# Performance work log

Hardware: AMD Instinct MI355X
Metric: run time of the kernel (lower is better)

Reference implementation:

```python
import jax, jax.numpy as jnp
import numpy as np

B, S, D, H = 2, 2048, 1024, 16
HD = D // H
EPS = 1e-5


def layer_norm(x, g, b):
    m = jnp.mean(x, axis=-1, keepdims=True)
    v = jnp.mean(jnp.square(x - m), axis=-1, keepdims=True)
    return (x - m) * jax.lax.rsqrt(v + EPS) * g + b


def setup_inputs() -> dict:
    key = jax.random.key(0)
    ks = jax.random.split(key, 16)
    s = 0.02
    x = jax.random.normal(ks[0], (B, S, D), dtype=jnp.float32)
    mask = jax.random.randint(ks[1], (1, 1, S, S), 0, 2, dtype=jnp.int32)
    return {
        "x": x,
        "mask": mask,
        "Wq": jax.random.normal(ks[2], (D, D), jnp.float32) * s,
        "Wk": jax.random.normal(ks[3], (D, D), jnp.float32) * s,
        "Wv": jax.random.normal(ks[4], (D, D), jnp.float32) * s,
        "Wo": jax.random.normal(ks[5], (D, D), jnp.float32) * s,
        "bo": jax.random.normal(ks[6], (D,), jnp.float32) * s,
        "ln1_g": jnp.ones((D,), jnp.float32),
        "ln1_b": jnp.zeros((D,), jnp.float32),
        "W1": jax.random.normal(ks[7], (D, 4 * D), jnp.float32) * s,
        "b1": jax.random.normal(ks[8], (4 * D,), jnp.float32) * s,
        "W2": jax.random.normal(ks[9], (4 * D, D), jnp.float32) * s,
        "b2": jax.random.normal(ks[10], (D,), jnp.float32) * s,
        "ln2_g": jnp.ones((D,), jnp.float32),
        "ln2_b": jnp.zeros((D,), jnp.float32),
    }


def reference(x, mask, Wq, Wk, Wv, Wo, bo, ln1_g, ln1_b, W1, b1, W2, b2, ln2_g, ln2_b):
    # --- multi-head attention (dropout = identity in eval) ---
    q = (x @ Wq).reshape(B, S, H, HD)
    k = (x @ Wk).reshape(B, S, H, HD)
    v = (x @ Wv).reshape(B, S, H, HD)
    scores = jnp.einsum("bshd,bthd->bhst", q, k) / jnp.sqrt(jnp.float32(HD))
    scores = jnp.where(mask == 1, jnp.float32(-1e9), scores)
    p = jax.nn.softmax(scores, axis=-1)
    o = jnp.einsum("bhst,bthd->bshd", p, v).reshape(B, S, D)
    attn_out = o @ Wo + bo
    # --- residual with norm on the branch (note: norm applied to attn output) ---
    x = x + layer_norm(attn_out, ln1_g, ln1_b)
    # --- FFN: gelu after fc1 AND after fc2 (as in source) ---
    h = jax.nn.gelu(x @ W1 + b1, approximate=False)
    h = jax.nn.gelu(h @ W2 + b2, approximate=False)
    x = x + layer_norm(h, ln2_g, ln2_b)
    return x
```

## Files before the change

### kernel.cpp

```cpp
#include <hip/hip_runtime.h>
#include <hip/hip_bf16.h>
#include <cstdint>

#define BB 2
#define SS 2048
#define DD 1024
#define HH 16
#define HDIM 64
#define MROWS (BB*SS)

typedef __bf16 bf16;
using bf16x8 = __bf16 __attribute__((ext_vector_type(8)));
using bf16x4 = __bf16 __attribute__((ext_vector_type(4)));
using bf16x2 = __bf16 __attribute__((ext_vector_type(2)));
using f32x4  = float __attribute__((ext_vector_type(4)));

__device__ __forceinline__ float gelu_exact(float x) {
    return 0.5f * x * (1.f + erff(x * 0.70710678118654752f));
}

__device__ __forceinline__ void stage16(const bf16* g, bf16* lds_chunk_base, int lane) {
#if __has_builtin(__builtin_amdgcn_global_load_lds)
    __builtin_amdgcn_global_load_lds((const __attribute__((address_space(1))) void*)g,
                                     (__attribute__((address_space(3))) void*)lds_chunk_base,
                                     16, 0, 0);
#else
    *(bf16x8*)(lds_chunk_base + lane * 8) = *(const bf16x8*)g;
#endif
}

__global__ __launch_bounds__(256) void prep_kernel(
    const float* __restrict__ x, bf16* __restrict__ x_b,
    const int* __restrict__ mask, unsigned long long* __restrict__ maskb,
    const float* __restrict__ Wq, const float* __restrict__ Wk,
    const float* __restrict__ Wv, const float* __restrict__ Wo,
    const float* __restrict__ W1, const float* __restrict__ W2,
    bf16* __restrict__ Wqkv_t, bf16* __restrict__ Wo_t,
    bf16* __restrict__ W1_t, bf16* __restrict__ W2_t) {
    const int bid = blockIdx.x;
    if (bid < 4096) {
        int i = bid * 256 + threadIdx.x;
        float4 v = ((const float4*)x)[i];
        bf16x4 o;
        o[0] = (bf16)v.x; o[1] = (bf16)v.y; o[2] = (bf16)v.z; o[3] = (bf16)v.w;
        *(bf16x4*)(x_b + (size_t)i * 4) = o;
        return;
    }
    if (bid < 20480) {
        int gid = (bid - 4096) * 256 + threadIdx.x;
        int mv = mask[gid];
        unsigned long long bal = __ballot(mv == 1);
        if ((threadIdx.x & 63) == 0) maskb[gid >> 6] = bal;
        return;
    }
    int t = bid - 20480;
    const float* W; bf16* Wt; int K, N, bx, by;
    if (t < 4096) {
        int wsel = t >> 10;
        int tt = t & 1023;
        W  = (wsel == 0) ? Wq : (wsel == 1) ? Wk : (wsel == 2) ? Wv : Wo;
        Wt = (wsel == 3) ? Wo_t : (Wqkv_t + (size_t)wsel * 1024 * 1024);
        K = 1024; N = 1024; bx = (tt & 31) * 32; by = (tt >> 5) * 32;
    } else if (t < 8192) {
        int tt = t - 4096;
        W = W1; Wt = W1_t; K = 1024; N = 4096;
        bx = (tt & 127) * 32; by = (tt >> 7) * 32;
    } else {
        int tt = t - 8192;
        W = W2; Wt = W2_t; K = 4096; N = 1024;
        bx = (tt & 31) * 32; by = (tt >> 5) * 32;
    }
    __shared__ float tile[32][33];
    int tx = threadIdx.x & 31;
    int ty = threadIdx.x >> 5;
#pragma unroll
    for (int j = 0; j < 4; ++j)
        tile[ty + j * 8][tx] = W[(size_t)(by + ty + j * 8) * N + bx + tx];
    __syncthreads();
#pragma unroll
    for (int j = 0; j < 4; ++j)
        Wt[(size_t)(bx + ty + j * 8) * K + by + tx] = (bf16)tile[tx][ty + j * 8];
}

template <int EPI>
__global__ __launch_bounds__(256, 3) void gemm_bt(const bf16* __restrict__ A,
                                                  const bf16* __restrict__ Bt,
                                                  void* __restrict__ C,
                                                  void* __restrict__ C2,
                                                  const float* __restrict__ bias,
                                                  int M, int N, int K, int ldk) {
    __shared__ __align__(16) bf16 As[128 * 64];
    __shared__ __align__(16) bf16 Bs[128 * 64];
    const int tid  = threadIdx.x;
    const int lane = tid & 63;
    const int wave = tid >> 6;
    const int l16  = lane & 15;
    const int quad = lane >> 4;
    const int wm = wave >> 1, wn = wave & 1;
    const int m0 = blockIdx.y * 128, n0 = blockIdx.x * 128;
    const int z  = blockIdx.z;
    A  += (size_t)z * K;
    Bt += (size_t)z * K;

    f32x4 acc[4][4];
#pragma unroll
    for (int i = 0; i < 4; ++i)
#pragma unroll
        for (int j = 0; j < 4; ++j) acc[i][j] = (f32x4){0.f, 0.f, 0.f, 0.f};

    const int nsteps = K >> 6;
    for (int kt = 0; kt < nsteps; ++kt) {
        const int kbase = kt << 6;
#pragma unroll
        for (int c = 0; c < 4; ++c) {
            int chunk = wave * 4 + c;
            int gi = chunk * 64 + lane;
            int m  = gi >> 3;
            int cp = gi & 7;
            int g  = cp ^ (m & 7);
            stage16(A  + (size_t)(m0 + m) * ldk + kbase + g * 8, As + chunk * 512, lane);
            stage16(Bt + (size_t)(n0 + m) * ldk + kbase + g * 8, Bs + chunk * 512, lane);
        }
        __syncthreads();
#pragma unroll
        for (int ks = 0; ks < 2; ++ks) {
            bf16x8 af[4], bfr[4];
#pragma unroll
            for (int i = 0; i < 4; ++i) {
                int m = wm * 64 + i * 16 + l16;
                int g = ks * 4 + quad;
                af[i]  = *(const bf16x8*)(As + m * 64 + ((g ^ (m & 7)) * 8));
                int n = wn * 64 + i * 16 + l16;
                bfr[i] = *(const bf16x8*)(Bs + n * 64 + ((g ^ (n & 7)) * 8));
            }
#pragma unroll
            for (int i = 0; i < 4; ++i)
#pragma unroll
                for (int j = 0; j < 4; ++j)
                    acc[i][j] = __builtin_amdgcn_mfma_f32_16x16x32_bf16(af[i], bfr[j], acc[i][j], 0, 0, 0);
        }
        __syncthreads();
    }

    float* Cz = (EPI == 4) ? (z ? (float*)C2 : (float*)C) : nullptr;
#pragma unroll
    for (int i = 0; i < 4; ++i) {
        int row = m0 + wm * 64 + i * 16 + quad * 4;
#pragma unroll
        for (int j = 0; j < 4; ++j) {
            int col = n0 + wn * 64 + j * 16 + l16;
            float bv = (EPI == 2) ? bias[col] : 0.f;
#pragma unroll
            for (int r = 0; r < 4; ++r) {
                float v = acc[i][j][r];
                if (EPI == 2) v = gelu_exact(v + bv);
                size_t idx = (size_t)(row + r) * N + col;
                if (EPI == 4) Cz[idx] = v;
                else          ((bf16*)C)[idx] = (bf16)v;
            }
        }
    }
}

__global__ __launch_bounds__(256) void flash_attn(const bf16* __restrict__ qkv,
                                                  const unsigned long long* __restrict__ maskb,
                                                  bf16* __restrict__ o) {
    __shared__ __align__(16) bf16 Ks[128 * 64];
    __shared__ __align__(16) bf16 Vts[64 * 136];
    const int tid  = threadIdx.x;
    const int lane = tid & 63;
    const int wave = tid >> 6;
    const int l16  = lane & 15;
    const int quad = lane >> 4;
    const int bh = blockIdx.y;
    const int b = bh >> 4, h = bh & 15;
    const int q0 = blockIdx.x * 64;
    const size_t rowb = (size_t)b * SS;
    const float SCL = 0.18033688011112042f;

    const size_t qrow = (rowb + q0 + wave * 16 + l16) * 3072 + h * 64;
    bf16x8 qf[2];
    qf[0] = *(const bf16x8*)(qkv + qrow + quad * 8);
    qf[1] = *(const bf16x8*)(qkv + qrow + 32 + quad * 8);

    f32x4 oacc[4];
#pragma unroll
    for (int d = 0; d < 4; ++d) oacc[d] = (f32x4){0.f, 0.f, 0.f, 0.f};
    float lsum = 0.f;
    const int mrow32 = (q0 + wave * 16 + l16) * 32;

    const int vt_tc = (lane >> 4) * 32 + ((lane >> 1) & 3) * 8 + ((lane >> 3) & 1) * 4 + 2 * (lane & 1);

    for (int kt = 0; kt < SS / 128; ++kt) {
        const int t0 = kt * 128;
        ulonglong2 mw = *(const ulonglong2*)(maskb + mrow32 + kt * 2);
        __syncthreads();
#pragma unroll
        for (int c = 0; c < 4; ++c) {
            int chunk = wave * 4 + c;
            int gi = chunk * 64 + lane;
            int t  = gi >> 3;
            int cp = gi & 7;
            int g  = cp ^ (t & 7);
            stage16(qkv + (rowb + t0 + t) * 3072 + 1024 + h * 64 + g * 8, Ks + chunk * 512, lane);
        }
#pragma unroll
        for (int c = 0; c < 2; ++c) {
            int d8 = (wave + 4 * c) * 8;
            const bf16* vg = qkv + (rowb + t0 + 2 * lane) * 3072 + 2048 + h * 64 + d8;
            bf16x8 v0 = *(const bf16x8*)(vg);
            bf16x8 v1 = *(const bf16x8*)(vg + 3072);
#pragma unroll
            for (int j = 0; j < 8; ++j) {
                bf16x2 pr; pr[0] = v0[j]; pr[1] = v1[j];
                *(bf16x2*)(Vts + (d8 + j) * 136 + vt_tc) = pr;
            }
        }
        __syncthreads();

        f32x4 st[8];
#pragma unroll
        for (int tg = 0; tg < 8; ++tg) {
            int tl = tg * 16 + l16;
            bf16x8 a0 = *(const bf16x8*)(Ks + tl * 64 + ((quad       ^ (tl & 7)) * 8));
            bf16x8 a1 = *(const bf16x8*)(Ks + tl * 64 + (((4 + quad) ^ (tl & 7)) * 8));
            f32x4 s = (f32x4){0.f, 0.f, 0.f, 0.f};
            s = __builtin_amdgcn_mfma_f32_16x16x32_bf16(a0, qf[0], s, 0, 0, 0);
            s = __builtin_amdgcn_mfma_f32_16x16x32_bf16(a1, qf[1], s, 0, 0, 0);
            st[tg] = s;
        }
        unsigned long long s0 = mw.x >> (quad * 4);
        unsigned long long s1 = mw.y >> (quad * 4);
        bf16x8 pva[4];
#pragma unroll
        for (int tg = 0; tg < 8; ++tg) {
            unsigned int bits = (unsigned int)(((tg < 4) ? s0 : s1) >> ((tg & 3) * 16));
#pragma unroll
            for (int r = 0; r < 4; ++r) {
                float p = __builtin_amdgcn_exp2f(st[tg][r] * SCL);
                p = ((bits >> r) & 1u) ? 0.f : p;
                lsum += p;
                pva[tg >> 1][(tg & 1) * 4 + r] = (bf16)p;
            }
        }
#pragma unroll
        for (int kc = 0; kc < 4; ++kc) {
#pragma unroll
            for (int dg = 0; dg < 4; ++dg) {
                bf16x8 bfrag = *(const bf16x8*)(Vts + (dg * 16 + l16) * 136 + kc * 32 + quad * 8);
                oacc[dg] = __builtin_amdgcn_mfma_f32_16x16x32_bf16(pva[kc], bfrag, oacc[dg], 0, 0, 0);
            }
        }
    }

    lsum += __shfl_xor(lsum, 16, 64);
    lsum += __shfl_xor(lsum, 32, 64);
#pragma unroll
    for (int r = 0; r < 4; ++r) {
        float lr = __shfl(lsum, quad * 4 + r, 64);
        float inv_l = 1.f / lr;
        bf16* orow = o + (rowb + q0 + wave * 16 + quad * 4 + r) * DD + h * 64;
#pragma unroll
        for (int dg = 0; dg < 4; ++dg)
            orow[dg * 16 + l16] = (bf16)(oacc[dg][r] * inv_l);
    }
}

template <bool GELU, bool WB16>
__global__ __launch_bounds__(256) void ln_fused(const float* __restrict__ resid,
                                                const float* __restrict__ p0,
                                                const float* __restrict__ p1,
                                                const float* __restrict__ bias,
                                                const float* __restrict__ g,
                                                const float* __restrict__ bb,
                                                float* __restrict__ outf,
                                                bf16* __restrict__ outb) {
    const int row = blockIdx.x;
    const int tid = threadIdx.x;
    const size_t base = (size_t)row * DD + tid * 4;
    float4 a0 = *(const float4*)(p0 + base);
    float4 a1 = *(const float4*)(p1 + base);
    float4 bz = *(const float4*)(bias + tid * 4);
    float ax = a0.x + a1.x + bz.x;
    float ay = a0.y + a1.y + bz.y;
    float az = a0.z + a1.z + bz.z;
    float aw = a0.w + a1.w + bz.w;
    if (GELU) { ax = gelu_exact(ax); ay = gelu_exact(ay); az = gelu_exact(az); aw = gelu_exact(aw); }
    float s1 = ax + ay + az + aw;
    float s2 = ax * ax + ay * ay + az * az + aw * aw;
#pragma unroll
    for (int off = 32; off; off >>= 1) {
        s1 += __shfl_xor(s1, off, 64);
        s2 += __shfl_xor(s2, off, 64);
    }
    __shared__ float red[8];
    if ((tid & 63) == 0) { red[(tid >> 6) * 2] = s1; red[(tid >> 6) * 2 + 1] = s2; }
    __syncthreads();
    s1 = red[0] + red[2] + red[4] + red[6];
    s2 = red[1] + red[3] + red[5] + red[7];
    float mean = s1 * (1.f / DD);
    float var  = s2 * (1.f / DD) - mean * mean;
    float rs = rsqrtf(var + 1e-5f);
    float4 gv = *(const float4*)(g + tid * 4);
    float4 bv = *(const float4*)(bb + tid * 4);
    float4 rv = *(const float4*)(resid + base);
    float y0 = rv.x + (ax - mean) * rs * gv.x + bv.x;
    float y1 = rv.y + (ay - mean) * rs * gv.y + bv.y;
    float y2 = rv.z + (az - mean) * rs * gv.z + bv.z;
    float y3 = rv.w + (aw - mean) * rs * gv.w + bv.w;
    float4 yo = make_float4(y0, y1, y2, y3);
    *(float4*)(outf + base) = yo;
    if (WB16) {
        bf16x4 ob;
        ob[0] = (bf16)y0; ob[1] = (bf16)y1; ob[2] = (bf16)y2; ob[3] = (bf16)y3;
        *(bf16x4*)(outb + base) = ob;
    }
}

extern "C" void kernel_launch(void* const* d_in, const int* in_sizes, int n_in,
                              void* d_out, int out_size, void* d_ws, size_t ws_size,
                              hipStream_t stream) {
    const float* x    = (const float*)d_in[0];
    const int*   mask = (const int*)d_in[1];
    const float* Wq   = (const float*)d_in[2];
    const float* Wk   = (const float*)d_in[3];
    const float* Wv   = (const float*)d_in[4];
    const float* Wo   = (const float*)d_in[5];
    const float* bo   = (const float*)d_in[6];
    const float* ln1g = (const float*)d_in[7];
    const float* ln1b = (const float*)d_in[8];
    const float* W1   = (const float*)d_in[9];
    const float* b1   = (const float*)d_in[10];
    const float* W2   = (const float*)d_in[11];
    const float* b2   = (const float*)d_in[12];
    const float* ln2g = (const float*)d_in[13];
    const float* ln2b = (const float*)d_in[14];

    char* w = (char*)d_ws;
    bf16* Wqkv_t = (bf16*)w; w += (size_t)3072 * 1024 * 2;
    bf16* Wo_t   = (bf16*)w; w += (size_t)1024 * 1024 * 2;
    bf16* W1_t   = (bf16*)w; w += (size_t)4096 * 1024 * 2;
    bf16* W2_t   = (bf16*)w; w += (size_t)1024 * 4096 * 2;
    bf16* x_b    = (bf16*)w; w += (size_t)MROWS * DD * 2;
    bf16* qkv    = (bf16*)w; w += (size_t)MROWS * 3072 * 2;
    float* R     = (float*)w; w += (size_t)MROWS * DD * 8;
    float* x1_f  = (float*)w; w += (size_t)MROWS * DD * 4;
    unsigned long long* maskb = (unsigned long long*)w; w += (size_t)SS * 32 * 8;
    bf16* o_b  = x_b;
    bf16* x1_b = x_b;
    float* op0 = R;
    float* op1 = R + (size_t)MROWS * DD;
    bf16*  h_b = (bf16*)R;
    float* fp0 = (float*)d_out;
    float* fp1 = (float*)qkv;

    prep_kernel<<<32768, 256, 0, stream>>>(x, x_b, mask, maskb,
                                           Wq, Wk, Wv, Wo, W1, W2,
                                           Wqkv_t, Wo_t, W1_t, W2_t);

    gemm_bt<0><<<dim3(24, 32, 1), 256, 0, stream>>>(x_b, Wqkv_t, qkv, nullptr, nullptr, MROWS, 3072, 1024, 1024);
    flash_attn<<<dim3(SS / 64, BB * HH), 256, 0, stream>>>(qkv, maskb, o_b);
    gemm_bt<4><<<dim3(8, 32, 2), 256, 0, stream>>>(o_b, Wo_t, op0, op1, nullptr, MROWS, 1024, 512, 1024);
    ln_fused<false, true><<<MROWS, 256, 0, stream>>>(x, op0, op1, bo, ln1g, ln1b, x1_f, x1_b);
    gemm_bt<2><<<dim3(32, 32, 1), 256, 0, stream>>>(x1_b, W1_t, h_b, nullptr, b1, MROWS, 4096, 1024, 1024);
    gemm_bt<4><<<dim3(8, 32, 2), 256, 0, stream>>>(h_b, W2_t, fp0, fp1, nullptr, MROWS, 1024, 2048, 4096);
    ln_fused<true, false><<<MROWS, 256, 0, stream>>>(x1_f, fp0, fp1, b2, ln2g, ln2b, (float*)d_out, nullptr);
}
```

Baseline: 390.7 us.

## Software-pipeline K/V loads through registers in flash attention and fold scale into Q

Global loads of the next K/V tile and mask words are issued into registers right after the barrier, so they overlap the current tile's MFMA and softmax work instead of stalling the LDS staging. The softmax scale is folded into Q once at load time, and the row sum is computed with an extra MFMA against a ones vector rather than scalar adds and shuffles. The change also adds wave priority hints around MFMA blocks and an occupancy hint in launch_bounds. The costs are higher register pressure from holding prefetched tiles, the loss of direct-to-LDS loads, and a small precision change from rounding the scaled Q to bf16. The row sum is now taken over the bf16-rounded probabilities rather than the fp32 values.

```diff
diff --git a/kernel.cpp b/kernel.cpp
--- a/kernel.cpp
+++ b/kernel.cpp
@@ -162,9 +162,9 @@
     }
 }
 
-__global__ __launch_bounds__(256) void flash_attn(const bf16* __restrict__ qkv,
-                                                  const unsigned long long* __restrict__ maskb,
-                                                  bf16* __restrict__ o) {
+__global__ __launch_bounds__(256, 4) void flash_attn(const bf16* __restrict__ qkv,
+                                                     const unsigned long long* __restrict__ maskb,
+                                                     bf16* __restrict__ o) {
     __shared__ __align__(16) bf16 Ks[128 * 64];
     __shared__ __align__(16) bf16 Vts[64 * 136];
     const int tid  = threadIdx.x;
@@ -180,45 +180,82 @@
 
     const size_t qrow = (rowb + q0 + wave * 16 + l16) * 3072 + h * 64;
     bf16x8 qf[2];
-    qf[0] = *(const bf16x8*)(qkv + qrow + quad * 8);
-    qf[1] = *(const bf16x8*)(qkv + qrow + 32 + quad * 8);
+    {
+        bf16x8 q0r = *(const bf16x8*)(qkv + qrow + quad * 8);
+        bf16x8 q1r = *(const bf16x8*)(qkv + qrow + 32 + quad * 8);
+#pragma unroll
+        for (int j = 0; j < 8; ++j) {
+            qf[0][j] = (bf16)((float)q0r[j] * SCL);
+            qf[1][j] = (bf16)((float)q1r[j] * SCL);
+        }
+    }
 
     f32x4 oacc[4];
 #pragma unroll
     for (int d = 0; d < 4; ++d) oacc[d] = (f32x4){0.f, 0.f, 0.f, 0.f};
-    float lsum = 0.f;
+    f32x4 lacc = (f32x4){0.f, 0.f, 0.f, 0.f};
     const int mrow32 = (q0 + wave * 16 + l16) * 32;
 
+    bf16x8 ones;
+#pragma unroll
+    for (int j = 0; j < 8; ++j) ones[j] = (bf16)1.0f;
+
     const int vt_tc = (lane >> 4) * 32 + ((lane >> 1) & 3) * 8 + ((lane >> 3) & 1) * 4 + 2 * (lane & 1);
 
+    int kst[4], ksg[4];
+#pragma unroll
+    for (int c = 0; c < 4; ++c) {
+        int gi = (wave * 4 + c) * 64 + lane;
+        kst[c] = gi >> 3;
+        ksg[c] = (gi & 7) ^ (kst[c] & 7);
+    }
+
+    bf16x8 kreg[4], vreg[4];
+    ulonglong2 mwreg;
+#pragma unroll
+    for (int c = 0; c < 4; ++c)
+        kreg[c] = *(const bf16x8*)(qkv + (rowb + kst[c]) * 3072 + 1024 + h * 64 + ksg[c] * 8);
+#pragma unroll
+    for (int c = 0; c < 2; ++c) {
+        const bf16* vg = qkv + (rowb + 2 * lane) * 3072 + 2048 + h * 64 + (wave + 4 * c) * 8;
+        vreg[2 * c]     = *(const bf16x8*)(vg);
+        vreg[2 * c + 1] = *(const bf16x8*)(vg + 3072);
+    }
+    mwreg = *(const ulonglong2*)(maskb + mrow32);
+
     for (int kt = 0; kt < SS / 128; ++kt) {
-        const int t0 = kt * 128;
-        ulonglong2 mw = *(const ulonglong2*)(maskb + mrow32 + kt * 2);
         __syncthreads();
 #pragma unroll
-        for (int c = 0; c < 4; ++c) {
-            int chunk = wave * 4 + c;
-            int gi = chunk * 64 + lane;
-            int t  = gi >> 3;
-            int cp = gi & 7;
-            int g  = cp ^ (t & 7);
-            stage16(qkv + (rowb + t0 + t) * 3072 + 1024 + h * 64 + g * 8, Ks + chunk * 512, lane);
-        }
+        for (int c = 0; c < 4; ++c)
+            *(bf16x8*)(Ks + (wave * 4 + c) * 512 + lane * 8) = kreg[c];
 #pragma unroll
         for (int c = 0; c < 2; ++c) {
             int d8 = (wave + 4 * c) * 8;
-            const bf16* vg = qkv + (rowb + t0 + 2 * lane) * 3072 + 2048 + h * 64 + d8;
-            bf16x8 v0 = *(const bf16x8*)(vg);
-            bf16x8 v1 = *(const bf16x8*)(vg + 3072);
 #pragma unroll
             for (int j = 0; j < 8; ++j) {
-                bf16x2 pr; pr[0] = v0[j]; pr[1] = v1[j];
+                bf16x2 pr; pr[0] = vreg[2 * c][j]; pr[1] = vreg[2 * c + 1][j];
                 *(bf16x2*)(Vts + (d8 + j) * 136 + vt_tc) = pr;
             }
         }
+        ulonglong2 mw = mwreg;
         __syncthreads();
 
+        if (kt + 1 < SS / 128) {
+            const int t0n = (kt + 1) * 128;
+#pragma unroll
+            for (int c = 0; c < 4; ++c)
+                kreg[c] = *(const bf16x8*)(qkv + (rowb + t0n + kst[c]) * 3072 + 1024 + h * 64 + ksg[c] * 8);
+#pragma unroll
+            for (int c = 0; c < 2; ++c) {
+                const bf16* vg = qkv + (rowb + t0n + 2 * lane) * 3072 + 2048 + h * 64 + (wave + 4 * c) * 8;
+                vreg[2 * c]     = *(const bf16x8*)(vg);
+                vreg[2 * c + 1] = *(const bf16x8*)(vg + 3072);
+            }
+            mwreg = *(const ulonglong2*)(maskb + mrow32 + (kt + 1) * 2);
+        }
+
         f32x4 st[8];
+        __builtin_amdgcn_s_setprio(1);
 #pragma unroll
         for (int tg = 0; tg < 8; ++tg) {
             int tl = tg * 16 + l16;
@@ -229,6 +266,8 @@
             s = __builtin_amdgcn_mfma_f32_16x16x32_bf16(a1, qf[1], s, 0, 0, 0);
             st[tg] = s;
         }
+        __builtin_amdgcn_s_setprio(0);
+
         unsigned long long s0 = mw.x >> (quad * 4);
         unsigned long long s1 = mw.y >> (quad * 4);
         bf16x8 pva[4];
@@ -237,12 +276,13 @@
             unsigned int bits = (unsigned int)(((tg < 4) ? s0 : s1) >> ((tg & 3) * 16));
 #pragma unroll
             for (int r = 0; r < 4; ++r) {
-                float p = __builtin_amdgcn_exp2f(st[tg][r] * SCL);
+                float p = __builtin_amdgcn_exp2f(st[tg][r]);
                 p = ((bits >> r) & 1u) ? 0.f : p;
-                lsum += p;
                 pva[tg >> 1][(tg & 1) * 4 + r] = (bf16)p;
             }
         }
+
+        __builtin_amdgcn_s_setprio(1);
 #pragma unroll
         for (int kc = 0; kc < 4; ++kc) {
 #pragma unroll
@@ -250,15 +290,14 @@
                 bf16x8 bfrag = *(const bf16x8*)(Vts + (dg * 16 + l16) * 136 + kc * 32 + quad * 8);
                 oacc[dg] = __builtin_amdgcn_mfma_f32_16x16x32_bf16(pva[kc], bfrag, oacc[dg], 0, 0, 0);
             }
-        }
-    }
-
-    lsum += __shfl_xor(lsum, 16, 64);
-    lsum += __shfl_xor(lsum, 32, 64);
+            lacc = __builtin_amdgcn_mfma_f32_16x16x32_bf16(pva[kc], ones, lacc, 0, 0, 0);
+        }
+        __builtin_amdgcn_s_setprio(0);
+    }
+
 #pragma unroll
     for (int r = 0; r < 4; ++r) {
-        float lr = __shfl(lsum, quad * 4 + r, 64);
-        float inv_l = 1.f / lr;
+        float inv_l = 1.f / lacc[r];
         bf16* orow = o + (rowb + q0 + wave * 16 + quad * 4 + r) * DD + h * 64;
 #pragma unroll
         for (int dg = 0; dg < 4; ++dg)
```

Result: faster. 377.7 us (-3.3%).
